# Optimization experiments

Hardware: AMD Instinct MI355X
Metric: run time of the kernel (lower is better)

Reference implementation:

```python
import jax, jax.numpy as jnp
import numpy as np

EPS_MSG = 1e-7   # GENConv eps added after ReLU on messages
LN_EPS = 1e-5    # torch LayerNorm default eps
N_NODES = 100000
N_EDGES = 1200000
NODE_DIM = 128
EDGE_DIM = 8
HID = 64
OUT_DIM = 112
L = 7            # num_layers


def layer_norm(x, g, b):
    mu = jnp.mean(x, axis=-1, keepdims=True)
    var = jnp.mean((x - mu) ** 2, axis=-1, keepdims=True)
    return (x - mu) * jax.lax.rsqrt(var + LN_EPS) * g + b


def setup_inputs() -> dict:
    key = jax.random.key(0)
    ks = jax.random.split(key, 10)
    return {
        "node_feats": jax.random.normal(ks[0], (N_NODES, NODE_DIM), jnp.float32),
        "edge_feats": jax.random.normal(ks[1], (N_EDGES, EDGE_DIM), jnp.float32),
        "src": jax.random.randint(ks[2], (N_EDGES,), 0, N_NODES, dtype=jnp.int32),
        "dst": jax.random.randint(ks[3], (N_EDGES,), 0, N_NODES, dtype=jnp.int32),
        "W_node": (jax.random.normal(ks[4], (NODE_DIM, HID), jnp.float32) * 0.05),
        "b_node": jnp.zeros((HID,), jnp.float32),
        "W_edge": (jax.random.normal(ks[5], (EDGE_DIM, HID), jnp.float32) * 0.05),
        "b_edge": jnp.zeros((HID,), jnp.float32),
        "betas": jnp.ones((L,), jnp.float32),  # learnable beta per GENConv, init 1.0
        "W1": (jax.random.normal(ks[6], (L, HID, 2 * HID), jnp.float32) * 0.05),
        "b1": jnp.zeros((L, 2 * HID), jnp.float32),
        "ln1_g": jnp.ones((L, 2 * HID), jnp.float32),
        "ln1_b": jnp.zeros((L, 2 * HID), jnp.float32),
        "W2": (jax.random.normal(ks[7], (L, 2 * HID, HID), jnp.float32) * 0.05),
        "b2": jnp.zeros((L, HID), jnp.float32),
        "norm_g": jnp.ones((L, HID), jnp.float32),   # DeepGCNLayer LayerNorm affine
        "norm_b": jnp.zeros((L, HID), jnp.float32),
        "W_out": (jax.random.normal(ks[8], (HID, OUT_DIM), jnp.float32) * 0.05),
        "b_out": jnp.zeros((OUT_DIM,), jnp.float32),
    }


def reference(node_feats, edge_feats, src, dst, W_node, b_node, W_edge, b_edge,
              betas, W1, b1, ln1_g, ln1_b, W2, b2, norm_g, norm_b, W_out, b_out):
    h = node_feats @ W_node + b_node        # [N, HID] node encoder
    eh = edge_feats @ W_edge + b_edge       # [E, HID] edge encoder
    for i in range(L):
        # DeepGCNLayer 'res+': x = dropout(relu(norm(h))); h = h + conv(x)
        # (dropout is identity in eval mode)
        x = jax.nn.relu(layer_norm(h, norm_g[i], norm_b[i]))
        # GENConv softmax aggregation with learnable beta
        m = jax.nn.relu(x[src] + eh) + EPS_MSG          # [E, HID] messages
        logits = m * betas[i]
        mx = jax.ops.segment_max(logits, dst, num_segments=N_NODES)
        e = jnp.exp(logits - mx[dst])
        s = jax.ops.segment_sum(e, dst, num_segments=N_NODES)
        a = e / s[dst]                                   # per-dst per-feature softmax
        agg = jax.ops.segment_sum(m * a, dst, num_segments=N_NODES)  # [N, HID]
        # GENConv MLP (2 layers, HID -> 2*HID -> HID, LayerNorm+ReLU in between)
        y = x + agg
        y = jax.nn.relu(layer_norm(y @ W1[i] + b1[i], ln1_g[i], ln1_b[i]))
        y = y @ W2[i] + b2[i]
        h = h + y
    # final: activation(norm_of_layer0(h)) -> dropout(identity) -> output linear
    h = jax.nn.relu(layer_norm(h, norm_g[0], norm_b[0]))
    return h @ W_out + b_out
```

## Files before the change

kernel.cpp:

```cpp
#include <hip/hip_runtime.h>
#include <hip/hip_bf16.h>

#define N_NODES 100000
#define N_PAD   100032
#define N_EDGES 1200000
#define HID 64
#define OUT_DIM 112
#define NLAYERS 7

static constexpr int SCAN_BLOCKS = (N_NODES + 255) / 256;

typedef __attribute__((ext_vector_type(8))) short short8v;
typedef __attribute__((ext_vector_type(4))) float f32x4;
typedef unsigned int uint;
typedef unsigned short ushort;
typedef __attribute__((ext_vector_type(4))) uint uintx4;

__device__ __forceinline__ unsigned f2b(float f) {
    unsigned u = __builtin_bit_cast(unsigned, f);
    return (u + 0x7FFFu + ((u >> 16) & 1u)) >> 16;
}
__device__ __forceinline__ float blo(uint v) {
    return __builtin_bit_cast(float, (v & 0xFFFFu) << 16);
}
__device__ __forceinline__ float bhi(uint v) {
    return __builtin_bit_cast(float, v & 0xFFFF0000u);
}


__global__ __launch_bounds__(256) void k_rank(const int* __restrict__ dst, int* __restrict__ cnt,
                                              int* __restrict__ rank) {
    int e0 = (blockIdx.x * 256 + threadIdx.x) * 4;
    if (e0 + 3 < N_EDGES) {
        int4 d4 = *(const int4*)&dst[e0];
        int r0 = atomicAdd(&cnt[d4.x], 1);
        int r1 = atomicAdd(&cnt[d4.y], 1);
        int r2 = atomicAdd(&cnt[d4.z], 1);
        int r3 = atomicAdd(&cnt[d4.w], 1);
        *(int4*)&rank[e0] = make_int4(r0, r1, r2, r3);
    } else {
        for (int e = e0; e < N_EDGES; ++e) rank[e] = atomicAdd(&cnt[dst[e]], 1);
    }
}

__global__ __launch_bounds__(256) void k_scan_a(const int* __restrict__ cnt, int* __restrict__ inc,
                                                int* __restrict__ bsum) {
    __shared__ int lds[4];
    int i = blockIdx.x * 256 + threadIdx.x;
    int v = (i < N_NODES) ? cnt[i] : 0;
    int lane = threadIdx.x & 63, w = threadIdx.x >> 6;
    #pragma unroll
    for (int d = 1; d < 64; d <<= 1) {
        int u = __shfl_up(v, d, 64);
        if (lane >= d) v += u;
    }
    if (lane == 63) lds[w] = v;
    __syncthreads();
    int add = 0;
    for (int j = 0; j < w; ++j) add += lds[j];
    v += add;
    if (i < N_NODES) inc[i] = v;
    if (threadIdx.x == 255) bsum[blockIdx.x] = v;
}

__global__ __launch_bounds__(512) void k_scan_b(const int* __restrict__ bsum, int* __restrict__ boff, int nb) {
    __shared__ int lds[8];
    int t = threadIdx.x;
    int v0 = (t < nb) ? bsum[t] : 0;
    int v = v0;
    int lane = t & 63, w = t >> 6;
    #pragma unroll
    for (int d = 1; d < 64; d <<= 1) {
        int u = __shfl_up(v, d, 64);
        if (lane >= d) v += u;
    }
    if (lane == 63) lds[w] = v;
    __syncthreads();
    int add = 0;
    for (int j = 0; j < w; ++j) add += lds[j];
    boff[t] = v + add - v0;
}

__global__ __launch_bounds__(256) void k_scan_c(const int* __restrict__ inc, const int* __restrict__ boff,
                                                int* __restrict__ rp) {
    int i = blockIdx.x * 256 + threadIdx.x;
    if (i < N_NODES) {
        rp[i + 1] = inc[i] + boff[blockIdx.x];
        if (i == 0) rp[0] = 0;
    }
}

__global__ __launch_bounds__(256) void k_prep_w(const float* __restrict__ W1, const float* __restrict__ W2,
                                                const float* __restrict__ Wn, const float* __restrict__ Wo,
                                                short* __restrict__ W1T, short* __restrict__ W2T,
                                                short* __restrict__ WnT, short* __restrict__ WoT) {
    int t = blockIdx.x * 256 + threadIdx.x;
    if (t < NLAYERS * 8192) {
        int l = t >> 13, r = t & 8191;
        int o1 = r >> 6, k1 = r & 63;
        W1T[t] = (short)f2b(W1[l * 8192 + k1 * 128 + o1]);
        int o2 = r >> 7, k2 = r & 127;
        W2T[t] = (short)f2b(W2[l * 8192 + k2 * 64 + o2]);
        if (t < 8192) {
            int o = t >> 7, k = t & 127;
            WnT[t] = (short)f2b(Wn[k * 64 + o]);
        }
        if (t < OUT_DIM * 64) {
            int o = t >> 6, k = t & 63;
            WoT[t] = (short)f2b(Wo[k * OUT_DIM + o]);
        }
    }
}


__global__ __launch_bounds__(256) void k_node_enc_mfma(
    const float* __restrict__ nf, const short* __restrict__ WnT, const float* __restrict__ bn,
    const float* __restrict__ g, const float* __restrict__ b,
    float* __restrict__ h, ushort* __restrict__ xb) {
    __shared__ __align__(16) short Wns[8192];
    __shared__ __align__(16) short nfs[4][2048];
    int tid = threadIdx.x, lane = tid & 63, w = tid >> 6;

    {
        const int4* gp = (const int4*)WnT;
        for (int u = tid; u < 1024; u += 256) {
            int byte = u * 16;
            int off = byte ^ (((byte >> 8) & 7) << 4);
            *(int4*)((char*)Wns + off) = gp[u];
        }
    }
    int nbase = blockIdx.x * 64 + w * 16;
    #pragma unroll
    for (int it = 0; it < 8; ++it) {
        int idx = it * 256 + lane * 4;
        int node = idx >> 7, k0 = idx & 127;
        int gn = nbase + node;
        float4 v = (gn < N_NODES) ? *(const float4*)&nf[(size_t)gn * 128 + k0]
                                  : make_float4(0.f, 0.f, 0.f, 0.f);
        uint2 pk;
        pk.x = f2b(v.x) | (f2b(v.y) << 16);
        pk.y = f2b(v.z) | (f2b(v.w) << 16);
        int boff = (node * 256 + k0 * 2) ^ ((node & 7) << 4);
        *(uint2*)((char*)nfs[w] + boff) = pk;
    }
    __syncthreads();

    int cg = lane >> 4, cl = lane & 15;
    float bv[4], gv[4], bbv[4];
    #pragma unroll
    for (int t = 0; t < 4; ++t) {
        bv[t] = bn[t * 16 + cl]; gv[t] = g[t * 16 + cl]; bbv[t] = b[t * 16 + cl];
    }
    f32x4 c[4];
    #pragma unroll
    for (int t = 0; t < 4; ++t) c[t] = (f32x4){bv[t], bv[t], bv[t], bv[t]};
    #pragma unroll
    for (int s = 0; s < 4; ++s) {
        int aoff = (cl * 256 + s * 64 + cg * 16) ^ ((cl & 7) << 4);
        short8v af = *(const short8v*)((char*)nfs[w] + aoff);
        #pragma unroll
        for (int t = 0; t < 4; ++t) {
            int o = t * 16 + cl;
            int boff = (o * 256 + s * 64 + cg * 16) ^ ((o & 7) << 4);
            short8v bfv = *(const short8v*)((char*)Wns + boff);
            c[t] = __builtin_amdgcn_mfma_f32_16x16x32_bf16(af, bfv, c[t], 0, 0, 0);
        }
    }
    float s2[4] = {0, 0, 0, 0}, q2[4] = {0, 0, 0, 0};
    #pragma unroll
    for (int t = 0; t < 4; ++t)
        #pragma unroll
        for (int r = 0; r < 4; ++r) {
            int node = nbase + cg * 4 + r, o = t * 16 + cl;
            h[(size_t)node * 64 + o] = c[t][r];
            s2[r] += c[t][r]; q2[r] += c[t][r] * c[t][r];
        }
    #pragma unroll
    for (int r = 0; r < 4; ++r)
        #pragma unroll
        for (int d = 1; d < 16; d <<= 1) {
            s2[r] += __shfl_xor(s2[r], d, 16);
            q2[r] += __shfl_xor(q2[r], d, 16);
        }
    #pragma unroll
    for (int r = 0; r < 4; ++r) {
        float mu = s2[r] * (1.f / 64.f);
        float var = q2[r] * (1.f / 64.f) - mu * mu;
        float rv = rsqrtf(var + 1e-5f);
        #pragma unroll
        for (int t = 0; t < 4; ++t) {
            int node = nbase + cg * 4 + r, o = t * 16 + cl;
            float xv = fmaxf((c[t][r] - mu) * rv * gv[t] + bbv[t], 0.f);
            xb[(size_t)node * 64 + o] = (ushort)f2b(xv);
        }
    }
}

__global__ __launch_bounds__(256) void k_edge_enc(
    const float* __restrict__ ef, const float* __restrict__ We, const float* __restrict__ be,
    const int* __restrict__ dst, const int* __restrict__ rank, const int* __restrict__ rp,
    const int* __restrict__ src, int* __restrict__ ssrc, ushort* __restrict__ eh) {
    __shared__ float efs[2048];
    int tid = threadIdx.x, lane = tid & 63, w = tid >> 6;
    float wreg[8];
    #pragma unroll
    for (int k = 0; k < 8; ++k) wreg[k] = We[k * 64 + lane];
    float bv = be[lane];
    int base = blockIdx.x * 256;
    if (base >= N_EDGES) return;
    #pragma unroll
    for (int u = 0; u < 2; ++u) {
        int idx = u * 1024 + tid * 4;
        size_t gidx = (size_t)base * 8 + idx;
        float4 v = (gidx < (size_t)N_EDGES * 8) ? *(const float4*)&ef[gidx]
                                                : make_float4(0.f, 0.f, 0.f, 0.f);
        *(float4*)&efs[idx] = v;
    }
    int ge0 = base + w * 64 + lane;
    int myp = -1;
    if (ge0 < N_EDGES) {
        myp = rp[dst[ge0]] + rank[ge0];
        __builtin_nontemporal_store(src[ge0], &ssrc[myp]);
    }
    __syncthreads();
    #pragma unroll 4
    for (int j = 0; j < 64; ++j) {
        int p = __shfl(myp, j, 64);
        if (p >= 0) {
            float4 a = *(const float4*)&efs[(w * 64 + j) * 8];
            float4 b = *(const float4*)&efs[(w * 64 + j) * 8 + 4];
            float acc = bv;
            acc = fmaf(a.x, wreg[0], acc); acc = fmaf(a.y, wreg[1], acc);
            acc = fmaf(a.z, wreg[2], acc); acc = fmaf(a.w, wreg[3], acc);
            acc = fmaf(b.x, wreg[4], acc); acc = fmaf(b.y, wreg[5], acc);
            acc = fmaf(b.z, wreg[6], acc); acc = fmaf(b.w, wreg[7], acc);
            __builtin_nontemporal_store((ushort)f2b(acc), &eh[(size_t)p * 64 + lane]);
        }
    }
}


__global__ __launch_bounds__(256) void k_agg(
    const ushort* __restrict__ xb, const ushort* __restrict__ eh,
    const int* __restrict__ ssrc, const int* __restrict__ rp,
    const float* __restrict__ betas, int layer, ushort* __restrict__ xab) {
    int lane = threadIdx.x & 63;
    int n = blockIdx.x * 8 + (threadIdx.x >> 6) * 2 + (lane >> 5);
    int slot = (lane >> 3) & 3;
    int f8 = lane & 7;
    float beta = betas[layer];
    int r0 = rp[n], r1 = rp[n + 1];
    float S[8], T[8];
    #pragma unroll
    for (int c = 0; c < 8; ++c) { S[c] = 0.f; T[c] = 0.f; }
    int i = r0 + slot;
    for (; i + 4 < r1; i += 8) {
        int sA = ssrc[i], sB = ssrc[i + 4];
        uint4 xvA = *(const uint4*)&xb[(size_t)sA * 64 + 8 * f8];
        uintx4 evA = __builtin_nontemporal_load((const uintx4*)&eh[(size_t)i * 64 + 8 * f8]);
        uint4 xvB = *(const uint4*)&xb[(size_t)sB * 64 + 8 * f8];
        uintx4 evB = __builtin_nontemporal_load((const uintx4*)&eh[(size_t)(i + 4) * 64 + 8 * f8]);
        float mA[8], mB[8];
        mA[0] = fmaxf(blo(xvA.x) + blo(evA[0]), 1e-7f);
        mA[1] = fmaxf(bhi(xvA.x) + bhi(evA[0]), 1e-7f);
        mA[2] = fmaxf(blo(xvA.y) + blo(evA[1]), 1e-7f);
        mA[3] = fmaxf(bhi(xvA.y) + bhi(evA[1]), 1e-7f);
        mA[4] = fmaxf(blo(xvA.z) + blo(evA[2]), 1e-7f);
        mA[5] = fmaxf(bhi(xvA.z) + bhi(evA[2]), 1e-7f);
        mA[6] = fmaxf(blo(xvA.w) + blo(evA[3]), 1e-7f);
        mA[7] = fmaxf(bhi(xvA.w) + bhi(evA[3]), 1e-7f);
        mB[0] = fmaxf(blo(xvB.x) + blo(evB[0]), 1e-7f);
        mB[1] = fmaxf(bhi(xvB.x) + bhi(evB[0]), 1e-7f);
        mB[2] = fmaxf(blo(xvB.y) + blo(evB[1]), 1e-7f);
        mB[3] = fmaxf(bhi(xvB.y) + bhi(evB[1]), 1e-7f);
        mB[4] = fmaxf(blo(xvB.z) + blo(evB[2]), 1e-7f);
        mB[5] = fmaxf(bhi(xvB.z) + bhi(evB[2]), 1e-7f);
        mB[6] = fmaxf(blo(xvB.w) + blo(evB[3]), 1e-7f);
        mB[7] = fmaxf(bhi(xvB.w) + bhi(evB[3]), 1e-7f);
        #pragma unroll
        for (int c = 0; c < 8; ++c) {
            float pA = __expf(mA[c] * beta);
            float pB = __expf(mB[c] * beta);
            S[c] += pA + pB;
            T[c] += mA[c] * pA + mB[c] * pB;
        }
    }
    for (; i < r1; i += 4) {
        int s0 = ssrc[i];
        uint4 xv = *(const uint4*)&xb[(size_t)s0 * 64 + 8 * f8];
        uintx4 ev = __builtin_nontemporal_load((const uintx4*)&eh[(size_t)i * 64 + 8 * f8]);
        float m[8];
        m[0] = fmaxf(blo(xv.x) + blo(ev[0]), 1e-7f);
        m[1] = fmaxf(bhi(xv.x) + bhi(ev[0]), 1e-7f);
        m[2] = fmaxf(blo(xv.y) + blo(ev[1]), 1e-7f);
        m[3] = fmaxf(bhi(xv.y) + bhi(ev[1]), 1e-7f);
        m[4] = fmaxf(blo(xv.z) + blo(ev[2]), 1e-7f);
        m[5] = fmaxf(bhi(xv.z) + bhi(ev[2]), 1e-7f);
        m[6] = fmaxf(blo(xv.w) + blo(ev[3]), 1e-7f);
        m[7] = fmaxf(bhi(xv.w) + bhi(ev[3]), 1e-7f);
        #pragma unroll
        for (int c = 0; c < 8; ++c) {
            float p = __expf(m[c] * beta);
            S[c] += p;
            T[c] += m[c] * p;
        }
    }
    #pragma unroll
    for (int c = 0; c < 8; ++c) {
        #pragma unroll
        for (int d = 8; d <= 16; d <<= 1) {
            S[c] += __shfl_xor(S[c], d, 64);
            T[c] += __shfl_xor(T[c], d, 64);
        }
    }
    if (slot == 0) {
        bool has = r1 > r0;
        float a[8];
        #pragma unroll
        for (int c = 0; c < 8; ++c) a[c] = has ? (T[c] / S[c]) : 0.f;
        uint4 xv = *(const uint4*)&xb[(size_t)n * 64 + 8 * f8];
        uint4 pk;
        pk.x = f2b(blo(xv.x) + a[0]) | (f2b(bhi(xv.x) + a[1]) << 16);
        pk.y = f2b(blo(xv.y) + a[2]) | (f2b(bhi(xv.y) + a[3]) << 16);
        pk.z = f2b(blo(xv.z) + a[4]) | (f2b(bhi(xv.z) + a[5]) << 16);
        pk.w = f2b(blo(xv.w) + a[6]) | (f2b(bhi(xv.w) + a[7]) << 16);
        *(uint4*)&xab[(size_t)n * 64 + 8 * f8] = pk;
    }
}

__global__ __launch_bounds__(256) void k_mlp_mfma(
    const ushort* __restrict__ xab, const short* __restrict__ W1T, const float* __restrict__ b1,
    const float* __restrict__ g1, const float* __restrict__ bt1,
    const short* __restrict__ W2T, const float* __restrict__ b2,
    const float* __restrict__ ng, const float* __restrict__ nb,
    float* __restrict__ h, ushort* __restrict__ xbout) {
    __shared__ __align__(16) short W1s[8192];
    __shared__ __align__(16) short W2s[8192];
    __shared__ __align__(16) short xas[4][1024];
    __shared__ __align__(16) short t1s[4][2048];
    int tid = threadIdx.x;
    int lane = tid & 63, w = tid >> 6;

    {
        const int4* g1p = (const int4*)W1T;
        const int4* g2p = (const int4*)W2T;
        for (int u = tid; u < 1024; u += 256) {
            int byte = u * 16;
            int off1 = byte ^ ((((byte >> 7) & 7)) << 4);
            *(int4*)((char*)W1s + off1) = g1p[u];
            int off2 = byte ^ ((((byte >> 8) & 7)) << 4);
            *(int4*)((char*)W2s + off2) = g2p[u];
        }
    }
    int nbase = blockIdx.x * 64 + w * 16;
    #pragma unroll
    for (int it = 0; it < 2; ++it) {
        int idx = it * 512 + lane * 8;
        int node = idx >> 6, k0 = idx & 63;
        int4 v = *(const int4*)&xab[(size_t)(nbase + node) * 64 + k0];
        int boff = (node * 128 + k0 * 2) ^ ((node & 7) << 4);
        *(int4*)((char*)xas[w] + boff) = v;
    }
    __syncthreads();

    int cg = lane >> 4;
    int cl = lane & 15;
    float b1v[8], g1v[8], t1bv[8];
    #pragma unroll
    for (int t = 0; t < 8; ++t) {
        b1v[t] = b1[t * 16 + cl]; g1v[t] = g1[t * 16 + cl]; t1bv[t] = bt1[t * 16 + cl];
    }
    f32x4 c1[8];
    #pragma unroll
    for (int t = 0; t < 8; ++t) c1[t] = (f32x4){b1v[t], b1v[t], b1v[t], b1v[t]};
    #pragma unroll
    for (int s = 0; s < 2; ++s) {
        int aoff = (cl * 128 + s * 64 + cg * 16) ^ ((cl & 7) << 4);
        short8v af = *(const short8v*)((char*)xas[w] + aoff);
        #pragma unroll
        for (int t = 0; t < 8; ++t) {
            int o = t * 16 + cl;
            int boff = (o * 128 + s * 64 + cg * 16) ^ ((o & 7) << 4);
            short8v bfv = *(const short8v*)((char*)W1s + boff);
            c1[t] = __builtin_amdgcn_mfma_f32_16x16x32_bf16(af, bfv, c1[t], 0, 0, 0);
        }
    }
    float sum[4] = {0, 0, 0, 0}, sq[4] = {0, 0, 0, 0};
    #pragma unroll
    for (int t = 0; t < 8; ++t)
        #pragma unroll
        for (int r = 0; r < 4; ++r) { sum[r] += c1[t][r]; sq[r] += c1[t][r] * c1[t][r]; }
    #pragma unroll
    for (int r = 0; r < 4; ++r)
        #pragma unroll
        for (int d = 1; d < 16; d <<= 1) {
            sum[r] += __shfl_xor(sum[r], d, 16);
            sq[r] += __shfl_xor(sq[r], d, 16);
        }
    float mu[4], rs[4];
    #pragma unroll
    for (int r = 0; r < 4; ++r) {
        mu[r] = sum[r] * (1.f / 128.f);
        float var = sq[r] * (1.f / 128.f) - mu[r] * mu[r];
        rs[r] = rsqrtf(var + 1e-5f);
    }
    #pragma unroll
    for (int t = 0; t < 8; ++t)
        #pragma unroll
        for (int r = 0; r < 4; ++r) {
            float v = fmaxf((c1[t][r] - mu[r]) * rs[r] * g1v[t] + t1bv[t], 0.f);
            int node = cg * 4 + r, o = t * 16 + cl;
            int boff = (node * 256 + o * 2) ^ ((node & 7) << 4);
            *(short*)((char*)t1s[w] + boff) = (short)f2b(v);
        }
    __syncthreads();
    float b2v[4], ngv[4], nbv[4];
    #pragma unroll
    for (int t = 0; t < 4; ++t) {
        b2v[t] = b2[t * 16 + cl]; ngv[t] = ng[t * 16 + cl]; nbv[t] = nb[t * 16 + cl];
    }
    f32x4 c2[4];
    #pragma unroll
    for (int t = 0; t < 4; ++t) c2[t] = (f32x4){b2v[t], b2v[t], b2v[t], b2v[t]};
    #pragma unroll
    for (int s = 0; s < 4; ++s) {
        int aoff = (cl * 256 + s * 64 + cg * 16) ^ ((cl & 7) << 4);
        short8v af = *(const short8v*)((char*)t1s[w] + aoff);
        #pragma unroll
        for (int t = 0; t < 4; ++t) {
            int o = t * 16 + cl;
            int boff = (o * 256 + s * 64 + cg * 16) ^ ((o & 7) << 4);
            short8v bfv = *(const short8v*)((char*)W2s + boff);
            c2[t] = __builtin_amdgcn_mfma_f32_16x16x32_bf16(af, bfv, c2[t], 0, 0, 0);
        }
    }
    float hv[4][4];
    #pragma unroll
    for (int t = 0; t < 4; ++t)
        #pragma unroll
        for (int r = 0; r < 4; ++r) {
            int node = nbase + cg * 4 + r, o = t * 16 + cl;
            float v = h[(size_t)node * 64 + o] + c2[t][r];
            h[(size_t)node * 64 + o] = v;
            hv[t][r] = v;
        }
    float s2[4] = {0, 0, 0, 0}, q2[4] = {0, 0, 0, 0};
    #pragma unroll
    for (int t = 0; t < 4; ++t)
        #pragma unroll
        for (int r = 0; r < 4; ++r) { s2[r] += hv[t][r]; q2[r] += hv[t][r] * hv[t][r]; }
    #pragma unroll
    for (int r = 0; r < 4; ++r)
        #pragma unroll
        for (int d = 1; d < 16; d <<= 1) {
            s2[r] += __shfl_xor(s2[r], d, 16);
            q2[r] += __shfl_xor(q2[r], d, 16);
        }
    #pragma unroll
    for (int r = 0; r < 4; ++r) {
        float m2 = s2[r] * (1.f / 64.f);
        float var = q2[r] * (1.f / 64.f) - m2 * m2;
        float rv = rsqrtf(var + 1e-5f);
        #pragma unroll
        for (int t = 0; t < 4; ++t) {
            int node = nbase + cg * 4 + r, o = t * 16 + cl;
            float xv = fmaxf((hv[t][r] - m2) * rv * ngv[t] + nbv[t], 0.f);
            xbout[(size_t)node * 64 + o] = (ushort)f2b(xv);
        }
    }
}

__global__ __launch_bounds__(256) void k_out_mfma(
    const ushort* __restrict__ xb, const short* __restrict__ WoT, const float* __restrict__ bo,
    float* __restrict__ out) {
    __shared__ __align__(16) short Wos[OUT_DIM * 64];
    __shared__ __align__(16) short xs[4][1024];
    int tid = threadIdx.x, lane = tid & 63, w = tid >> 6;

    {
        const int4* gp = (const int4*)WoT;
        for (int u = tid; u < OUT_DIM * 8; u += 256) {
            int byte = u * 16;
            int off = byte ^ (((byte >> 7) & 7) << 4);
            *(int4*)((char*)Wos + off) = gp[u];
        }
    }
    int nbase = blockIdx.x * 64 + w * 16;
    #pragma unroll
    for (int it = 0; it < 2; ++it) {
        int idx = it * 512 + lane * 8;
        int node = idx >> 6, k0 = idx & 63;
        int4 v = *(const int4*)&xb[(size_t)(nbase + node) * 64 + k0];
        int boff = (node * 128 + k0 * 2) ^ ((node & 7) << 4);
        *(int4*)((char*)xs[w] + boff) = v;
    }
    __syncthreads();

    int cg = lane >> 4, cl = lane & 15;
    f32x4 c[7];
    #pragma unroll
    for (int t = 0; t < 7; ++t) {
        float bv = bo[t * 16 + cl];
        c[t] = (f32x4){bv, bv, bv, bv};
    }
    #pragma unroll
    for (int s = 0; s < 2; ++s) {
        int aoff = (cl * 128 + s * 64 + cg * 16) ^ ((cl & 7) << 4);
        short8v af = *(const short8v*)((char*)xs[w] + aoff);
        #pragma unroll
        for (int t = 0; t < 7; ++t) {
            int o = t * 16 + cl;
            int boff = (o * 128 + s * 64 + cg * 16) ^ ((o & 7) << 4);
            short8v bfv = *(const short8v*)((char*)Wos + boff);
            c[t] = __builtin_amdgcn_mfma_f32_16x16x32_bf16(af, bfv, c[t], 0, 0, 0);
        }
    }
    #pragma unroll
    for (int t = 0; t < 7; ++t)
        #pragma unroll
        for (int r = 0; r < 4; ++r) {
            int node = nbase + cg * 4 + r;
            if (node < N_NODES) out[(size_t)node * OUT_DIM + t * 16 + cl] = c[t][r];
        }
}


extern "C" void kernel_launch(void* const* d_in, const int* in_sizes, int n_in,
                              void* d_out, int out_size, void* d_ws, size_t ws_size,
                              hipStream_t stream) {
    (void)in_sizes; (void)n_in; (void)out_size; (void)ws_size;
    const float* node_feats = (const float*)d_in[0];
    const float* edge_feats = (const float*)d_in[1];
    const int*   src        = (const int*)d_in[2];
    const int*   dst        = (const int*)d_in[3];
    const float* W_node     = (const float*)d_in[4];
    const float* b_node     = (const float*)d_in[5];
    const float* W_edge     = (const float*)d_in[6];
    const float* b_edge     = (const float*)d_in[7];
    const float* betas      = (const float*)d_in[8];
    const float* W1         = (const float*)d_in[9];
    const float* b1         = (const float*)d_in[10];
    const float* ln1_g      = (const float*)d_in[11];
    const float* ln1_b      = (const float*)d_in[12];
    const float* W2         = (const float*)d_in[13];
    const float* b2         = (const float*)d_in[14];
    const float* norm_g     = (const float*)d_in[15];
    const float* norm_b     = (const float*)d_in[16];
    const float* W_out      = (const float*)d_in[17];
    const float* b_out      = (const float*)d_in[18];
    float* out = (float*)d_out;

    char* p = (char*)d_ws;
    auto carve = [&](size_t bytes) {
        char* r = p;
        p += (bytes + 255) & ~(size_t)255;
        return r;
    };
    float*  h    = (float*)carve((size_t)N_PAD * 64 * sizeof(float));
    ushort* xb   = (ushort*)carve((size_t)N_PAD * 64 * sizeof(short));
    ushort* xab  = (ushort*)carve((size_t)N_PAD * 64 * sizeof(short));
    ushort* eh   = (ushort*)carve((size_t)N_EDGES * 64 * sizeof(short));
    int* rp   = (int*)carve((size_t)(N_NODES + 1) * sizeof(int));
    int* nxt  = (int*)carve((size_t)N_NODES * sizeof(int));
    int* inc  = (int*)carve((size_t)N_NODES * sizeof(int));
    int* ssrc = (int*)carve((size_t)N_EDGES * sizeof(int));
    int* rank = (int*)carve((size_t)N_EDGES * sizeof(int));
    int* bsum = (int*)carve(512 * sizeof(int));
    int* boff = (int*)carve(512 * sizeof(int));
    short* W1T = (short*)carve((size_t)NLAYERS * 8192 * sizeof(short));
    short* W2T = (short*)carve((size_t)NLAYERS * 8192 * sizeof(short));
    short* WnT = (short*)carve((size_t)8192 * sizeof(short));
    short* WoT = (short*)carve((size_t)OUT_DIM * 64 * sizeof(short));

    hipMemsetAsync(nxt, 0, (size_t)N_NODES * sizeof(int), stream);
    k_rank<<<(N_EDGES / 4 + 255) / 256, 256, 0, stream>>>(dst, nxt, rank);
    k_scan_a<<<SCAN_BLOCKS, 256, 0, stream>>>(nxt, inc, bsum);
    k_scan_b<<<1, 512, 0, stream>>>(bsum, boff, SCAN_BLOCKS);
    k_scan_c<<<SCAN_BLOCKS, 256, 0, stream>>>(inc, boff, rp);

    k_prep_w<<<(NLAYERS * 8192 + 255) / 256, 256, 0, stream>>>(W1, W2, W_node, W_out,
                                                               W1T, W2T, WnT, WoT);
    k_node_enc_mfma<<<N_PAD / 64, 256, 0, stream>>>(node_feats, WnT, b_node, norm_g, norm_b, h, xb);
    k_edge_enc<<<(N_EDGES + 255) / 256, 256, 0, stream>>>(edge_feats, W_edge, b_edge,
                                                          dst, rank, rp, src, ssrc, eh);

    for (int i = 0; i < NLAYERS; ++i) {
        int ni = (i + 1 < NLAYERS) ? (i + 1) : 0;
        k_agg<<<N_NODES / 8, 256, 0, stream>>>(xb, eh, ssrc, rp, betas, i, xab);
        k_mlp_mfma<<<N_PAD / 64, 256, 0, stream>>>(xab, W1T + i * 8192, b1 + i * 128,
                                                   ln1_g + i * 128, ln1_b + i * 128,
                                                   W2T + i * 8192, b2 + i * 64,
                                                   norm_g + ni * 64, norm_b + ni * 64,
                                                   h, xb);
    }

    k_out_mfma<<<N_PAD / 64, 256, 0, stream>>>(xb, WoT, b_out, out);
}
```

Before: 727.9 us.

## Recompute edge encoding inside aggregation instead of materializing 64-wide edge embeddings

Replaces the precomputed bf16 edge-embedding tensor (E x 64) with a permuted bf16 copy of the raw 8-dim edge features, and recomputes the 8->64 edge linear inside the aggregation kernel every layer. This cuts the per-layer streamed edge bytes roughly eightfold, trading memory traffic for 64 extra FMAs per edge per lane plus 72 weight registers. The aggregation loop is also restructured from a two-edge unroll to a single-edge loop with software prefetch of the next src index and edge features. The higher register pressure may lower occupancy, and the edge encoding now uses bf16-rounded inputs.

```diff
diff --git a/kernel.cpp b/kernel.cpp
--- a/kernel.cpp
+++ b/kernel.cpp
@@ -196,113 +196,101 @@
     }
 }
 
-__global__ __launch_bounds__(256) void k_edge_enc(
-    const float* __restrict__ ef, const float* __restrict__ We, const float* __restrict__ be,
-    const int* __restrict__ dst, const int* __restrict__ rank, const int* __restrict__ rp,
-    const int* __restrict__ src, int* __restrict__ ssrc, ushort* __restrict__ eh) {
-    __shared__ float efs[2048];
-    int tid = threadIdx.x, lane = tid & 63, w = tid >> 6;
-    float wreg[8];
-    #pragma unroll
-    for (int k = 0; k < 8; ++k) wreg[k] = We[k * 64 + lane];
-    float bv = be[lane];
-    int base = blockIdx.x * 256;
-    if (base >= N_EDGES) return;
+__global__ __launch_bounds__(256) void k_perm(
+    const float* __restrict__ ef, const int* __restrict__ dst, const int* __restrict__ rank,
+    const int* __restrict__ rp, const int* __restrict__ src,
+    int* __restrict__ ssrc, ushort* __restrict__ efb) {
+    int e0 = (blockIdx.x * 256 + threadIdx.x) * 2;
     #pragma unroll
     for (int u = 0; u < 2; ++u) {
-        int idx = u * 1024 + tid * 4;
-        size_t gidx = (size_t)base * 8 + idx;
-        float4 v = (gidx < (size_t)N_EDGES * 8) ? *(const float4*)&ef[gidx]
-                                                : make_float4(0.f, 0.f, 0.f, 0.f);
-        *(float4*)&efs[idx] = v;
-    }
-    int ge0 = base + w * 64 + lane;
-    int myp = -1;
-    if (ge0 < N_EDGES) {
-        myp = rp[dst[ge0]] + rank[ge0];
-        __builtin_nontemporal_store(src[ge0], &ssrc[myp]);
-    }
-    __syncthreads();
-    #pragma unroll 4
-    for (int j = 0; j < 64; ++j) {
-        int p = __shfl(myp, j, 64);
-        if (p >= 0) {
-            float4 a = *(const float4*)&efs[(w * 64 + j) * 8];
-            float4 b = *(const float4*)&efs[(w * 64 + j) * 8 + 4];
-            float acc = bv;
-            acc = fmaf(a.x, wreg[0], acc); acc = fmaf(a.y, wreg[1], acc);
-            acc = fmaf(a.z, wreg[2], acc); acc = fmaf(a.w, wreg[3], acc);
-            acc = fmaf(b.x, wreg[4], acc); acc = fmaf(b.y, wreg[5], acc);
-            acc = fmaf(b.z, wreg[6], acc); acc = fmaf(b.w, wreg[7], acc);
-            __builtin_nontemporal_store((ushort)f2b(acc), &eh[(size_t)p * 64 + lane]);
+        int e = e0 + u;
+        if (e < N_EDGES) {
+            int p = rp[dst[e]] + rank[e];
+            __builtin_nontemporal_store(src[e], &ssrc[p]);
+            float4 a = *(const float4*)&ef[(size_t)e * 8];
+            float4 b = *(const float4*)&ef[(size_t)e * 8 + 4];
+            uintx4 pk;
+            pk[0] = f2b(a.x) | (f2b(a.y) << 16);
+            pk[1] = f2b(a.z) | (f2b(a.w) << 16);
+            pk[2] = f2b(b.x) | (f2b(b.y) << 16);
+            pk[3] = f2b(b.z) | (f2b(b.w) << 16);
+            __builtin_nontemporal_store(pk, (uintx4*)&efb[(size_t)p * 8]);
         }
     }
 }
 
 
 __global__ __launch_bounds__(256) void k_agg(
-    const ushort* __restrict__ xb, const ushort* __restrict__ eh,
+    const ushort* __restrict__ xb, const ushort* __restrict__ efb,
     const int* __restrict__ ssrc, const int* __restrict__ rp,
+    const float* __restrict__ We, const float* __restrict__ be,
     const float* __restrict__ betas, int layer, ushort* __restrict__ xab) {
     int lane = threadIdx.x & 63;
     int n = blockIdx.x * 8 + (threadIdx.x >> 6) * 2 + (lane >> 5);
     int slot = (lane >> 3) & 3;
     int f8 = lane & 7;
     float beta = betas[layer];
+
+    float we[8][8];
+    #pragma unroll
+    for (int k = 0; k < 8; ++k) {
+        float4 a = *(const float4*)&We[k * 64 + f8 * 8];
+        float4 b = *(const float4*)&We[k * 64 + f8 * 8 + 4];
+        we[k][0] = a.x; we[k][1] = a.y; we[k][2] = a.z; we[k][3] = a.w;
+        we[k][4] = b.x; we[k][5] = b.y; we[k][6] = b.z; we[k][7] = b.w;
+    }
+    float bev[8];
+    {
+        float4 a = *(const float4*)&be[f8 * 8];
+        float4 b = *(const float4*)&be[f8 * 8 + 4];
+        bev[0] = a.x; bev[1] = a.y; bev[2] = a.z; bev[3] = a.w;
+        bev[4] = b.x; bev[5] = b.y; bev[6] = b.z; bev[7] = b.w;
+    }
+
     int r0 = rp[n], r1 = rp[n + 1];
     float S[8], T[8];
     #pragma unroll
     for (int c = 0; c < 8; ++c) { S[c] = 0.f; T[c] = 0.f; }
+
     int i = r0 + slot;
-    for (; i + 4 < r1; i += 8) {
-        int sA = ssrc[i], sB = ssrc[i + 4];
-        uint4 xvA = *(const uint4*)&xb[(size_t)sA * 64 + 8 * f8];
-        uintx4 evA = __builtin_nontemporal_load((const uintx4*)&eh[(size_t)i * 64 + 8 * f8]);
-        uint4 xvB = *(const uint4*)&xb[(size_t)sB * 64 + 8 * f8];
-        uintx4 evB = __builtin_nontemporal_load((const uintx4*)&eh[(size_t)(i + 4) * 64 + 8 * f8]);
-        float mA[8], mB[8];
-        mA[0] = fmaxf(blo(xvA.x) + blo(evA[0]), 1e-7f);
-        mA[1] = fmaxf(bhi(xvA.x) + bhi(evA[0]), 1e-7f);
-        mA[2] = fmaxf(blo(xvA.y) + blo(evA[1]), 1e-7f);
-        mA[3] = fmaxf(bhi(xvA.y) + bhi(evA[1]), 1e-7f);
-        mA[4] = fmaxf(blo(xvA.z) + blo(evA[2]), 1e-7f);
-        mA[5] = fmaxf(bhi(xvA.z) + bhi(evA[2]), 1e-7f);
-        mA[6] = fmaxf(blo(xvA.w) + blo(evA[3]), 1e-7f);
-        mA[7] = fmaxf(bhi(xvA.w) + bhi(evA[3]), 1e-7f);
-        mB[0] = fmaxf(blo(xvB.x) + blo(evB[0]), 1e-7f);
-        mB[1] = fmaxf(bhi(xvB.x) + bhi(evB[0]), 1e-7f);
-        mB[2] = fmaxf(blo(xvB.y) + blo(evB[1]), 1e-7f);
-        mB[3] = fmaxf(bhi(xvB.y) + bhi(evB[1]), 1e-7f);
-        mB[4] = fmaxf(blo(xvB.z) + blo(evB[2]), 1e-7f);
-        mB[5] = fmaxf(bhi(xvB.z) + bhi(evB[2]), 1e-7f);
-        mB[6] = fmaxf(blo(xvB.w) + blo(evB[3]), 1e-7f);
-        mB[7] = fmaxf(bhi(xvB.w) + bhi(evB[3]), 1e-7f);
-        #pragma unroll
-        for (int c = 0; c < 8; ++c) {
-            float pA = __expf(mA[c] * beta);
-            float pB = __expf(mB[c] * beta);
-            S[c] += pA + pB;
-            T[c] += mA[c] * pA + mB[c] * pB;
-        }
-    }
-    for (; i < r1; i += 4) {
-        int s0 = ssrc[i];
-        uint4 xv = *(const uint4*)&xb[(size_t)s0 * 64 + 8 * f8];
-        uintx4 ev = __builtin_nontemporal_load((const uintx4*)&eh[(size_t)i * 64 + 8 * f8]);
-        float m[8];
-        m[0] = fmaxf(blo(xv.x) + blo(ev[0]), 1e-7f);
-        m[1] = fmaxf(bhi(xv.x) + bhi(ev[0]), 1e-7f);
-        m[2] = fmaxf(blo(xv.y) + blo(ev[1]), 1e-7f);
-        m[3] = fmaxf(bhi(xv.y) + bhi(ev[1]), 1e-7f);
-        m[4] = fmaxf(blo(xv.z) + blo(ev[2]), 1e-7f);
-        m[5] = fmaxf(bhi(xv.z) + bhi(ev[2]), 1e-7f);
-        m[6] = fmaxf(blo(xv.w) + blo(ev[3]), 1e-7f);
-        m[7] = fmaxf(bhi(xv.w) + bhi(ev[3]), 1e-7f);
-        #pragma unroll
-        for (int c = 0; c < 8; ++c) {
-            float p = __expf(m[c] * beta);
-            S[c] += p;
-            T[c] += m[c] * p;
+    if (i < r1) {
+        int scur = ssrc[i];
+        uint4 ecur = *(const uint4*)&efb[(size_t)i * 8];
+        for (; i < r1; i += 4) {
+            int inext = i + 4;
+            int snxt = 0;
+            uint4 enxt = make_uint4(0, 0, 0, 0);
+            if (inext < r1) {
+                snxt = ssrc[inext];
+                enxt = *(const uint4*)&efb[(size_t)inext * 8];
+            }
+            uint4 xv = *(const uint4*)&xb[(size_t)scur * 64 + 8 * f8];
+            float ef8[8];
+            ef8[0] = blo(ecur.x); ef8[1] = bhi(ecur.x);
+            ef8[2] = blo(ecur.y); ef8[3] = bhi(ecur.y);
+            ef8[4] = blo(ecur.z); ef8[5] = bhi(ecur.z);
+            ef8[6] = blo(ecur.w); ef8[7] = bhi(ecur.w);
+            float acc[8];
+            #pragma unroll
+            for (int j = 0; j < 8; ++j) acc[j] = bev[j];
+            #pragma unroll
+            for (int k = 0; k < 8; ++k)
+                #pragma unroll
+                for (int j = 0; j < 8; ++j) acc[j] = fmaf(ef8[k], we[k][j], acc[j]);
+            float xf[8];
+            xf[0] = blo(xv.x); xf[1] = bhi(xv.x);
+            xf[2] = blo(xv.y); xf[3] = bhi(xv.y);
+            xf[4] = blo(xv.z); xf[5] = bhi(xv.z);
+            xf[6] = blo(xv.w); xf[7] = bhi(xv.w);
+            #pragma unroll
+            for (int c = 0; c < 8; ++c) {
+                float m = fmaxf(xf[c] + acc[c], 1e-7f);
+                float p = __expf(m * beta);
+                S[c] += p;
+                T[c] += m * p;
+            }
+            scur = snxt;
+            ecur = enxt;
         }
     }
     #pragma unroll
@@ -559,7 +547,7 @@
     float*  h    = (float*)carve((size_t)N_PAD * 64 * sizeof(float));
     ushort* xb   = (ushort*)carve((size_t)N_PAD * 64 * sizeof(short));
     ushort* xab  = (ushort*)carve((size_t)N_PAD * 64 * sizeof(short));
-    ushort* eh   = (ushort*)carve((size_t)N_EDGES * 64 * sizeof(short));
+    ushort* efb  = (ushort*)carve((size_t)N_EDGES * 8 * sizeof(short));
     int* rp   = (int*)carve((size_t)(N_NODES + 1) * sizeof(int));
     int* nxt  = (int*)carve((size_t)N_NODES * sizeof(int));
     int* inc  = (int*)carve((size_t)N_NODES * sizeof(int));
@@ -581,12 +569,13 @@
     k_prep_w<<<(NLAYERS * 8192 + 255) / 256, 256, 0, stream>>>(W1, W2, W_node, W_out,
                                                                W1T, W2T, WnT, WoT);
     k_node_enc_mfma<<<N_PAD / 64, 256, 0, stream>>>(node_feats, WnT, b_node, norm_g, norm_b, h, xb);
-    k_edge_enc<<<(N_EDGES + 255) / 256, 256, 0, stream>>>(edge_feats, W_edge, b_edge,
-                                                          dst, rank, rp, src, ssrc, eh);
+    k_perm<<<(N_EDGES / 2 + 255) / 256, 256, 0, stream>>>(edge_feats, dst, rank, rp, src,
+                                                          ssrc, efb);
 
     for (int i = 0; i < NLAYERS; ++i) {
         int ni = (i + 1 < NLAYERS) ? (i + 1) : 0;
-        k_agg<<<N_NODES / 8, 256, 0, stream>>>(xb, eh, ssrc, rp, betas, i, xab);
+        k_agg<<<N_NODES / 8, 256, 0, stream>>>(xb, efb, ssrc, rp, W_edge, b_edge,
+                                               betas, i, xab);
         k_mlp_mfma<<<N_PAD / 64, 256, 0, stream>>>(xab, W1T + i * 8192, b1 + i * 128,
                                                    ln1_g + i * 128, ln1_b + i * 128,
                                                    W2T + i * 8192, b2 + i * 64,
```

Measured after the change: 840.7 us. 15.5% more time.
